# Kernel tuning notes

Measured on AMD Instinct MI355X. Metric: run time of the kernel, lower is better.

The kernel has to match this reference:

```python
import jax, jax.numpy as jnp
import numpy as np

N, E, H = 100000, 1250000, 64
NF, EF = 16, 3
BN_EPS = 1e-5
HALF = H // 2


def setup_inputs() -> dict:
    key = jax.random.key(0)
    ks = jax.random.split(key, 24)
    g = lambda i, shape, s=0.05: jax.random.normal(ks[i], shape, dtype=jnp.float32) * s
    return {
        "x": jax.random.normal(ks[0], (N, NF), dtype=jnp.float32),
        "edge_attr": jax.random.normal(ks[1], (E, EF), dtype=jnp.float32),
        "edge_index": jax.random.randint(ks[2], (2, E), 0, N),
        "W_node": g(3, (NF, H)), "b_node": g(4, (H,)),
        "W_edge": g(5, (EF, H)), "b_edge": g(6, (H,)),
        "W_lin0": g(7, (H, H)), "b_lin0": g(8, (H,)),
        "W_att0": g(9, (2 * H + EF, 1)), "b_att0": g(10, (1,)),
        "W_sage_l": g(11, (H, H)), "b_sage_l": g(12, (H,)),
        "W_sage_r": g(13, (H, H)),
        "W_gcn": g(14, (H, H)), "b_gcn": g(15, (H,)),
        "bn_gamma": jnp.ones((3, H), jnp.float32),
        "bn_beta": jnp.zeros((3, H), jnp.float32),
        "W_r1": g(16, (H, H)), "b_r1": g(17, (H,)),
        "W_r2": g(18, (H, HALF)), "b_r2": g(19, (HALF,)),
        "W_r3": g(20, (HALF, 1)), "b_r3": g(21, (1,)),
    }


def _bn_eval(x, gamma, beta):
    # eval-mode BatchNorm1d with running_mean=0, running_var=1
    return x * (gamma / jnp.sqrt(1.0 + BN_EPS)) + beta


def _edge_att(h, src, dst, edge_attr, W, b, Wa, ba):
    # EdgeAttentionLayer: lin -> per-edge attention MLP -> scatter-add at dst
    h = h @ W + b                                   # [N,H]
    hi, hj = h[dst], h[src]                         # [E,H] gathers
    a = jnp.concatenate([hi, hj, edge_attr], -1) @ Wa + ba   # [E,1]
    a = jax.nn.sigmoid(jax.nn.leaky_relu(a, 0.01))
    return jax.ops.segment_sum(hj * a, dst, num_segments=N)


def _sage(h, src, dst, Wl, bl, Wr):
    # SAGEConv (mean aggregation): lin_l(mean_j x_j) + lin_r(x)
    agg = jax.ops.segment_sum(h[src], dst, num_segments=N)
    cnt = jax.ops.segment_sum(jnp.ones((src.shape[0], 1), h.dtype), dst, num_segments=N)
    mean = agg / jnp.maximum(cnt, 1.0)
    return mean @ Wl + bl + h @ Wr


def _gcn(h, src, dst, W, b):
    # GCNConv with self-loops and symmetric normalization
    hw = h @ W
    loop = jnp.arange(N)
    s = jnp.concatenate([src, loop])
    d = jnp.concatenate([dst, loop])
    deg = jax.ops.segment_sum(jnp.ones(s.shape[0], hw.dtype), d, num_segments=N)
    dis = jnp.where(deg > 0, jax.lax.rsqrt(jnp.maximum(deg, 1.0)), 0.0)
    norm = dis[s] * dis[d]                          # [E+N]
    return jax.ops.segment_sum(hw[s] * norm[:, None], d, num_segments=N) + b


def reference(x, edge_attr, edge_index, W_node, b_node, W_edge, b_edge,
              W_lin0, b_lin0, W_att0, b_att0, W_sage_l, b_sage_l, W_sage_r,
              W_gcn, b_gcn, bn_gamma, bn_beta, W_r1, b_r1, W_r2, b_r2, W_r3, b_r3):
    src, dst = edge_index[0], edge_index[1]
    h = x @ W_node + b_node
    _unused = edge_attr @ W_edge + b_edge  # computed in original forward, never used

    # layer 0: EdgeAttentionLayer + BN + ReLU (+residual; eval dropout = identity)
    ident = h
    h = _edge_att(h, src, dst, edge_attr, W_lin0, b_lin0, W_att0, b_att0)
    h = jax.nn.relu(_bn_eval(h, bn_gamma[0], bn_beta[0])) + ident

    # layer 1: SAGEConv
    ident = h
    h = _sage(h, src, dst, W_sage_l, b_sage_l, W_sage_r)
    h = jax.nn.relu(_bn_eval(h, bn_gamma[1], bn_beta[1])) + ident

    # layer 2: GCNConv
    ident = h
    h = _gcn(h, src, dst, W_gcn, b_gcn)
    h = jax.nn.relu(_bn_eval(h, bn_gamma[2], bn_beta[2])) + ident

    h = jax.nn.relu(h @ W_r1 + b_r1)
    h = jax.nn.relu(h @ W_r2 + b_r2)
    return h @ W_r3 + b_r3  # [N,1]
```

## Files before the change

kernel.cpp:

```cpp
#include <hip/hip_runtime.h>
#include <hip/hip_fp16.h>
#include <math.h>

#define NODES 100000
#define EDGES 1250000
#define HD 64
#define NFD 16
#define CHUNK 1024
#define NCHUNK ((NODES + CHUNK - 1) / CHUNK)
#define BN_INV 0.9999950000374996f
#define LP 65
#define SRCMASK 0x1FFFFu
#define WSCALE (1.0f / 32768.0f)


__global__ void k_hist(const int* __restrict__ ei, int* __restrict__ deg) {
  int e = blockIdx.x * blockDim.x + threadIdx.x;
  if (e < EDGES) atomicAdd(&deg[ei[EDGES + e]], 1);
}

__global__ void k_scan1(const int* __restrict__ deg, int* __restrict__ part) {
  __shared__ int lds[256];
  int t = threadIdx.x, b = blockIdx.x;
  int base = b * CHUNK + t * 4;
  int s = 0;
#pragma unroll
  for (int m = 0; m < 4; m++) { int i = base + m; if (i < NODES) s += deg[i]; }
  lds[t] = s; __syncthreads();
  for (int off = 128; off > 0; off >>= 1) {
    if (t < off) lds[t] += lds[t + off];
    __syncthreads();
  }
  if (t == 0) part[b] = lds[0];
}

__global__ void k_scan2(int* __restrict__ part) {
  if (threadIdx.x == 0 && blockIdx.x == 0) {
    int run = 0;
    for (int c = 0; c < NCHUNK; c++) { int v = part[c]; part[c] = run; run += v; }
  }
}

__global__ void k_scan3(const int* __restrict__ deg, const int* __restrict__ part,
                        int* __restrict__ rowptr, int* __restrict__ cur,
                        float* __restrict__ dis) {
  __shared__ int lds[256];
  int t = threadIdx.x, b = blockIdx.x;
  int base = b * CHUNK + t * 4;
  int dl[4]; int s = 0;
#pragma unroll
  for (int m = 0; m < 4; m++) { int i = base + m; dl[m] = (i < NODES) ? deg[i] : 0; s += dl[m]; }
  lds[t] = s; __syncthreads();
  for (int off = 1; off < 256; off <<= 1) {
    int add = (t >= off) ? lds[t - off] : 0;
    __syncthreads();
    lds[t] += add;
    __syncthreads();
  }
  int run = part[b] + lds[t] - s;
#pragma unroll
  for (int m = 0; m < 4; m++) {
    int i = base + m;
    if (i < NODES) {
      rowptr[i] = run; cur[i] = run;
      dis[i] = 1.0f / sqrtf((float)(dl[m] + 1));
    }
    run += dl[m];
  }
  if (b == 0 && t == 0) rowptr[NODES] = EDGES;
}

__global__ void k_fillatt(const int* __restrict__ ei, const float* __restrict__ ea,
                          const float* __restrict__ cvec, const float* __restrict__ dvec,
                          const float* __restrict__ Wa, const float* __restrict__ ba,
                          int* __restrict__ cur, uint* __restrict__ sa) {
  int e = blockIdx.x * blockDim.x + threadIdx.x;
  if (e >= EDGES) return;
  int s = ei[e], d = ei[EDGES + e];
  float alin = cvec[d] + dvec[s] + ea[3 * e] * Wa[128] + ea[3 * e + 1] * Wa[129] +
               ea[3 * e + 2] * Wa[130] + ba[0];
  float lr = alin >= 0.f ? alin : 0.01f * alin;
  float a = 1.f / (1.f + expf(-lr));
  uint q = min((int)(a * 32768.f + 0.5f), 32767);
  int p = atomicAdd(&cur[d], 1);
  sa[p] = (q << 17) | (uint)s;
}


__device__ __forceinline__ void store16h(__half* dst, const float* v) {
  uint u[8];
#pragma unroll
  for (int j = 0; j < 8; j++) {
    __half2 h = __float22half2_rn(make_float2(v[2 * j], v[2 * j + 1]));
    u[j] = *reinterpret_cast<uint*>(&h);
  }
  uint4* o = (uint4*)dst;
  o[0] = make_uint4(u[0], u[1], u[2], u[3]);
  o[1] = make_uint4(u[4], u[5], u[6], u[7]);
}

__device__ __forceinline__ float4 h4tof4(uint2 u) {
  float2 fa = __half22float2(*reinterpret_cast<__half2*>(&u.x));
  float2 fb = __half22float2(*reinterpret_cast<__half2*>(&u.y));
  return make_float4(fa.x, fa.y, fb.x, fb.y);
}

__device__ __forceinline__ void gstep(const __half* __restrict__ tab,
                                      const uint* __restrict__ sa,
                                      int m, int end, int last, int sub, int col,
                                      bool weighted,
                                      float4& A0, float4& A1, float4& A2, float4& A3) {
  int e0 = m + sub, e1 = e0 + 4, e2 = e0 + 8, e3 = e0 + 12;
  uint s0 = sa[min(e0, last)], s1 = sa[min(e1, last)];
  uint s2 = sa[min(e2, last)], s3 = sa[min(e3, last)];
  float w0 = (e0 < end) ? (weighted ? (float)(s0 >> 17) * WSCALE : 1.f) : 0.f;
  float w1 = (e1 < end) ? (weighted ? (float)(s1 >> 17) * WSCALE : 1.f) : 0.f;
  float w2 = (e2 < end) ? (weighted ? (float)(s2 >> 17) * WSCALE : 1.f) : 0.f;
  float w3 = (e3 < end) ? (weighted ? (float)(s3 >> 17) * WSCALE : 1.f) : 0.f;
  uint2 u0 = *((const uint2*)(tab + (size_t)(s0 & SRCMASK) * HD) + col);
  uint2 u1 = *((const uint2*)(tab + (size_t)(s1 & SRCMASK) * HD) + col);
  uint2 u2 = *((const uint2*)(tab + (size_t)(s2 & SRCMASK) * HD) + col);
  uint2 u3 = *((const uint2*)(tab + (size_t)(s3 & SRCMASK) * HD) + col);
  {
    float4 f = h4tof4(u0);
    A0.x = fmaf(w0, f.x, A0.x); A0.y = fmaf(w0, f.y, A0.y);
    A0.z = fmaf(w0, f.z, A0.z); A0.w = fmaf(w0, f.w, A0.w);
  }
  {
    float4 f = h4tof4(u1);
    A1.x = fmaf(w1, f.x, A1.x); A1.y = fmaf(w1, f.y, A1.y);
    A1.z = fmaf(w1, f.z, A1.z); A1.w = fmaf(w1, f.w, A1.w);
  }
  {
    float4 f = h4tof4(u2);
    A2.x = fmaf(w2, f.x, A2.x); A2.y = fmaf(w2, f.y, A2.y);
    A2.z = fmaf(w2, f.z, A2.z); A2.w = fmaf(w2, f.w, A2.w);
  }
  {
    float4 f = h4tof4(u3);
    A3.x = fmaf(w3, f.x, A3.x); A3.y = fmaf(w3, f.y, A3.y);
    A3.z = fmaf(w3, f.z, A3.z); A3.w = fmaf(w3, f.w, A3.w);
  }
}

__device__ __forceinline__ float4 red4(float4 a0, float4 a1, float4 a2, float4 a3) {
  float4 r;
  r.x = (a0.x + a1.x) + (a2.x + a3.x);
  r.y = (a0.y + a1.y) + (a2.y + a3.y);
  r.z = (a0.z + a1.z) + (a2.z + a3.z);
  r.w = (a0.w + a1.w) + (a2.w + a3.w);
#pragma unroll
  for (int off = 16; off <= 32; off <<= 1) {
    r.x += __shfl_xor(r.x, off); r.y += __shfl_xor(r.y, off);
    r.z += __shfl_xor(r.z, off); r.w += __shfl_xor(r.w, off);
  }
  return r;
}

#define AGG_BODY16(TABLE, WEIGHTED)                                              \
  float4 acc0 = make_float4(0.f, 0.f, 0.f, 0.f);                                 \
  float4 acc1 = make_float4(0.f, 0.f, 0.f, 0.f);                                 \
  float4 acc2 = make_float4(0.f, 0.f, 0.f, 0.f);                                 \
  float4 acc3 = make_float4(0.f, 0.f, 0.f, 0.f);                                 \
  int last = end - 1;                                                            \
  for (int m = start; m < end; m += 16)                                          \
    gstep(TABLE, sa, m, end, last, sub, col, WEIGHTED, acc0, acc1, acc2, acc3);  \
  float4 accr = red4(acc0, acc1, acc2, acc3);


__global__ __launch_bounds__(256) void k_lin0(
    const float* __restrict__ x,
    const float* __restrict__ Wn, const float* __restrict__ bn,
    const float* __restrict__ Wl, const float* __restrict__ bl,
    const float* __restrict__ Wa,
    float* __restrict__ hA, __half* __restrict__ hB16,
    float* __restrict__ cvec, float* __restrict__ dvec) {
  __shared__ float sh[64 * LP];
  __shared__ float sc[4][64], sd[4][64];
  int slot = threadIdx.x & 63;
  int cc = __builtin_amdgcn_readfirstlane(threadIdx.x >> 6);
  int c0 = cc * 16;
  int n0 = blockIdx.x * 64 + slot;
  bool valid = n0 < NODES;
  int n = valid ? n0 : NODES - 1;
  const float4* xr = (const float4*)(x + (size_t)n * NFD);
  float acc[16];
#pragma unroll
  for (int j = 0; j < 16; j++) acc[j] = bn[c0 + j];
#pragma unroll
  for (int q = 0; q < 4; q++) {
    float4 xa = xr[q];
    float xs[4] = {xa.x, xa.y, xa.z, xa.w};
#pragma unroll
    for (int t = 0; t < 4; t++)
#pragma unroll
      for (int j = 0; j < 16; j++)
        acc[j] = fmaf(xs[t], Wn[(q * 4 + t) * HD + c0 + j], acc[j]);
  }
#pragma unroll
  for (int j = 0; j < 16; j++) sh[slot * LP + c0 + j] = acc[j];
  if (valid) {
    float4* o = (float4*)(hA + (size_t)n * HD + c0);
    o[0] = make_float4(acc[0], acc[1], acc[2], acc[3]);
    o[1] = make_float4(acc[4], acc[5], acc[6], acc[7]);
    o[2] = make_float4(acc[8], acc[9], acc[10], acc[11]);
    o[3] = make_float4(acc[12], acc[13], acc[14], acc[15]);
  }
  __syncthreads();
  float a2[16];
#pragma unroll
  for (int j = 0; j < 16; j++) a2[j] = bl[c0 + j];
#pragma unroll 8
  for (int k = 0; k < 64; k++) {
    float hk = sh[slot * LP + k];
#pragma unroll
    for (int j = 0; j < 16; j++)
      a2[j] = fmaf(hk, Wl[k * HD + c0 + j], a2[j]);
  }
  float cn = 0.f, dn = 0.f;
#pragma unroll
  for (int j = 0; j < 16; j++) {
    cn = fmaf(a2[j], Wa[c0 + j], cn);
    dn = fmaf(a2[j], Wa[64 + c0 + j], dn);
  }
  if (valid) store16h(hB16 + (size_t)n * HD + c0, a2);
  sc[cc][slot] = cn;
  sd[cc][slot] = dn;
  __syncthreads();
  if (cc == 0 && valid) {
    cvec[n] = sc[0][slot] + sc[1][slot] + sc[2][slot] + sc[3][slot];
    dvec[n] = sd[0][slot] + sd[1][slot] + sd[2][slot] + sd[3][slot];
  }
}

__global__ __launch_bounds__(256) void k_agg_att(
    const uint* __restrict__ sa, const int* __restrict__ rowptr,
    const float* __restrict__ hA, const __half* __restrict__ hB16,
    const float* __restrict__ g, const float* __restrict__ bt,
    float* __restrict__ hC, __half* __restrict__ hC16) {
  int lane = threadIdx.x & 63;
  int node = __builtin_amdgcn_readfirstlane(blockIdx.x * 4 + (threadIdx.x >> 6));
  if (node >= NODES) return;
  int start = rowptr[node], end = rowptr[node + 1];
  int sub = lane >> 4, col = lane & 15;
  float4 gg = ((const float4*)g)[col];
  float4 bb = ((const float4*)bt)[col];
  float4 ha = *((const float4*)(hA + (size_t)node * HD) + col);
  AGG_BODY16(hB16, true)
  if (lane < 16) {
    float4 v;
    v.x = fmaxf(accr.x * (gg.x * BN_INV) + bb.x, 0.f) + ha.x;
    v.y = fmaxf(accr.y * (gg.y * BN_INV) + bb.y, 0.f) + ha.y;
    v.z = fmaxf(accr.z * (gg.z * BN_INV) + bb.z, 0.f) + ha.z;
    v.w = fmaxf(accr.w * (gg.w * BN_INV) + bb.w, 0.f) + ha.w;
    *((float4*)(hC + (size_t)node * HD) + col) = v;
    __half2 p0 = __float22half2_rn(make_float2(v.x, v.y));
    __half2 p1 = __float22half2_rn(make_float2(v.z, v.w));
    uint2 u;
    u.x = *reinterpret_cast<uint*>(&p0);
    u.y = *reinterpret_cast<uint*>(&p1);
    *((uint2*)(hC16 + (size_t)node * HD) + col) = u;
  }
}

__global__ __launch_bounds__(256) void k_msage(
    const uint* __restrict__ sa, const int* __restrict__ rowptr,
    const float* __restrict__ hC, const __half* __restrict__ hC16,
    const float* __restrict__ Wl, const float* __restrict__ bl,
    const float* __restrict__ Wr, const float* __restrict__ Wg,
    const float* __restrict__ g, const float* __restrict__ bt,
    const float* __restrict__ dis,
    float* __restrict__ hA, __half* __restrict__ hD16) {
  __shared__ float sh[64 * LP];
  int lane = threadIdx.x & 63;
  int wu = __builtin_amdgcn_readfirstlane(threadIdx.x >> 6);
  int sub = lane >> 4, col = lane & 15;
  int nbase = blockIdx.x * 64;
  for (int i = 0; i < 16; i++) {
    int slot = wu * 16 + i;
    int nn = min(nbase + slot, NODES - 1);
    int start = rowptr[nn], end = rowptr[nn + 1];
    float rdeg = 1.f / fmaxf((float)(end - start), 1.f);
    AGG_BODY16(hC16, false)
    if (lane < 16) {
      sh[slot * LP + col * 4 + 0] = accr.x * rdeg;
      sh[slot * LP + col * 4 + 1] = accr.y * rdeg;
      sh[slot * LP + col * 4 + 2] = accr.z * rdeg;
      sh[slot * LP + col * 4 + 3] = accr.w * rdeg;
    }
  }
  __syncthreads();
  int c0 = wu * 16;
  int n0 = nbase + lane;
  bool valid = n0 < NODES;
  int n = valid ? n0 : NODES - 1;
  const float4* cr = (const float4*)(hC + (size_t)n * HD);
  float acc[16];
#pragma unroll
  for (int j = 0; j < 16; j++) acc[j] = bl[c0 + j];
#pragma unroll 8
  for (int k = 0; k < 64; k++) {
    float mk = sh[lane * LP + k];
#pragma unroll
    for (int j = 0; j < 16; j++)
      acc[j] = fmaf(mk, Wl[k * HD + c0 + j], acc[j]);
  }
#pragma unroll 4
  for (int q = 0; q < 16; q++) {
    float4 ac = cr[q];
    float cs[4] = {ac.x, ac.y, ac.z, ac.w};
#pragma unroll
    for (int t = 0; t < 4; t++)
#pragma unroll
      for (int j = 0; j < 16; j++)
        acc[j] = fmaf(cs[t], Wr[(q * 4 + t) * HD + c0 + j], acc[j]);
  }
  float tv[16];
  {
    float4 r0 = cr[wu * 4 + 0], r1 = cr[wu * 4 + 1], r2 = cr[wu * 4 + 2], r3 = cr[wu * 4 + 3];
    float rv[16] = {r0.x, r0.y, r0.z, r0.w, r1.x, r1.y, r1.z, r1.w,
                    r2.x, r2.y, r2.z, r2.w, r3.x, r3.y, r3.z, r3.w};
#pragma unroll
    for (int j = 0; j < 16; j++)
      tv[j] = fmaxf(acc[j] * (g[c0 + j] * BN_INV) + bt[c0 + j], 0.f) + rv[j];
  }
  __syncthreads();
#pragma unroll
  for (int j = 0; j < 16; j++) sh[lane * LP + c0 + j] = tv[j];
  if (valid) {
    float4* o = (float4*)(hA + (size_t)n * HD + c0);
    o[0] = make_float4(tv[0], tv[1], tv[2], tv[3]);
    o[1] = make_float4(tv[4], tv[5], tv[6], tv[7]);
    o[2] = make_float4(tv[8], tv[9], tv[10], tv[11]);
    o[3] = make_float4(tv[12], tv[13], tv[14], tv[15]);
  }
  __syncthreads();
  float di = dis[n];
  float a2[16];
#pragma unroll
  for (int j = 0; j < 16; j++) a2[j] = 0.f;
#pragma unroll 8
  for (int k = 0; k < 64; k++) {
    float tk = sh[lane * LP + k];
#pragma unroll
    for (int j = 0; j < 16; j++)
      a2[j] = fmaf(tk, Wg[k * HD + c0 + j], a2[j]);
  }
#pragma unroll
  for (int j = 0; j < 16; j++) a2[j] *= di;
  if (valid) store16h(hD16 + (size_t)n * HD + c0, a2);
}

__global__ __launch_bounds__(256) void k_gcnreg(
    const uint* __restrict__ sa, const int* __restrict__ rowptr,
    const float* __restrict__ dis,
    const float* __restrict__ hA,
    const __half* __restrict__ hD16,
    const float* __restrict__ bg,
    const float* __restrict__ g, const float* __restrict__ bt,
    const float* __restrict__ W1, const float* __restrict__ b1,
    const float* __restrict__ W2, const float* __restrict__ b2,
    const float* __restrict__ W3, const float* __restrict__ b3,
    float* __restrict__ out) {
  __shared__ float sh[64 * LP];
  __shared__ float sred[4][64];
  int lane = threadIdx.x & 63;
  int wu = __builtin_amdgcn_readfirstlane(threadIdx.x >> 6);
  int sub = lane >> 4, col = lane & 15;
  int nbase = blockIdx.x * 64;
  float4 gg = ((const float4*)g)[col];
  float4 bb = ((const float4*)bt)[col];
  float4 bgv = ((const float4*)bg)[col];
  for (int i = 0; i < 16; i++) {
    int slot = wu * 16 + i;
    int nn = min(nbase + slot, NODES - 1);
    int start = rowptr[nn], end = rowptr[nn + 1];
    float di = dis[nn];
    float4 sv = h4tof4(*((const uint2*)(hD16 + (size_t)nn * HD) + col));
    float4 ha = *((const float4*)(hA + (size_t)nn * HD) + col);
    AGG_BODY16(hD16, false)
    if (lane < 16) {
      sh[slot * LP + col * 4 + 0] =
          fmaxf((di * (accr.x + sv.x) + bgv.x) * (gg.x * BN_INV) + bb.x, 0.f) + ha.x;
      sh[slot * LP + col * 4 + 1] =
          fmaxf((di * (accr.y + sv.y) + bgv.y) * (gg.y * BN_INV) + bb.y, 0.f) + ha.y;
      sh[slot * LP + col * 4 + 2] =
          fmaxf((di * (accr.z + sv.z) + bgv.z) * (gg.z * BN_INV) + bb.z, 0.f) + ha.z;
      sh[slot * LP + col * 4 + 3] =
          fmaxf((di * (accr.w + sv.w) + bgv.w) * (gg.w * BN_INV) + bb.w, 0.f) + ha.w;
    }
  }
  __syncthreads();
  int c0 = wu * 16;
  int n0 = nbase + lane;
  bool valid = n0 < NODES;
  int n = valid ? n0 : NODES - 1;
  float acc[16];
#pragma unroll
  for (int j = 0; j < 16; j++) acc[j] = b1[c0 + j];
#pragma unroll 8
  for (int k = 0; k < 64; k++) {
    float rk = sh[lane * LP + k];
#pragma unroll
    for (int j = 0; j < 16; j++)
      acc[j] = fmaf(rk, W1[k * HD + c0 + j], acc[j]);
  }
  float t1v[16];
#pragma unroll
  for (int j = 0; j < 16; j++) t1v[j] = fmaxf(acc[j], 0.f);
  __syncthreads();
#pragma unroll
  for (int j = 0; j < 16; j++) sh[lane * LP + c0 + j] = t1v[j];
  __syncthreads();
  int d0 = wu * 8;
  float a2[8];
#pragma unroll
  for (int j = 0; j < 8; j++) a2[j] = b2[d0 + j];
#pragma unroll 8
  for (int k = 0; k < 64; k++) {
    float tk = sh[lane * LP + k];
#pragma unroll
    for (int j = 0; j < 8; j++)
      a2[j] = fmaf(tk, W2[k * 32 + d0 + j], a2[j]);
  }
  float part = 0.f;
#pragma unroll
  for (int j = 0; j < 8; j++) part = fmaf(fmaxf(a2[j], 0.f), W3[d0 + j], part);
  sred[wu][lane] = part;
  __syncthreads();
  if (wu == 0 && valid)
    out[n] = sred[0][lane] + sred[1][lane] + sred[2][lane] + sred[3][lane] + b3[0];
}


extern "C" void kernel_launch(void* const* d_in, const int* in_sizes, int n_in,
                              void* d_out, int out_size, void* d_ws, size_t ws_size,
                              hipStream_t stream) {
  const float* x      = (const float*)d_in[0];
  const float* ea     = (const float*)d_in[1];
  const int*   ei     = (const int*)d_in[2];
  const float* W_node = (const float*)d_in[3];
  const float* b_node = (const float*)d_in[4];
  const float* W_lin0 = (const float*)d_in[7];
  const float* b_lin0 = (const float*)d_in[8];
  const float* W_att0 = (const float*)d_in[9];
  const float* b_att0 = (const float*)d_in[10];
  const float* W_sl   = (const float*)d_in[11];
  const float* b_sl   = (const float*)d_in[12];
  const float* W_sr   = (const float*)d_in[13];
  const float* W_gcn  = (const float*)d_in[14];
  const float* b_gcn  = (const float*)d_in[15];
  const float* bn_g   = (const float*)d_in[16];
  const float* bn_b   = (const float*)d_in[17];
  const float* W_r1   = (const float*)d_in[18];
  const float* b_r1   = (const float*)d_in[19];
  const float* W_r2   = (const float*)d_in[20];
  const float* b_r2   = (const float*)d_in[21];
  const float* W_r3   = (const float*)d_in[22];
  const float* b_r3   = (const float*)d_in[23];
  float* out = (float*)d_out;

  char* ws = (char*)d_ws;
  size_t o = 0;
  auto alloc = [&](size_t bytes) -> void* {
    void* p = ws + o;
    o += (bytes + 255) & ~(size_t)255;
    return p;
  };
  int*    deg    = (int*)alloc(NODES * 4);
  int*    rowptr = (int*)alloc((NODES + 1) * 4);
  int*    cur    = (int*)alloc(NODES * 4);
  int*    part   = (int*)alloc(256 * 4);
  uint*   sa     = (uint*)alloc((size_t)EDGES * 4);
  float*  hA     = (float*)alloc((size_t)NODES * HD * 4);
  float*  hC     = (float*)alloc((size_t)NODES * HD * 4);
  __half* hB16   = (__half*)alloc((size_t)NODES * HD * 2);
  __half* hC16   = (__half*)alloc((size_t)NODES * HD * 2);
  __half* hD16   = (__half*)alloc((size_t)NODES * HD * 2);
  float*  cvec   = (float*)alloc(NODES * 4);
  float*  dvec   = (float*)alloc(NODES * 4);
  float*  dis    = (float*)alloc(NODES * 4);
  (void)ws_size; (void)in_sizes; (void)n_in; (void)out_size;

  const int EB  = (EDGES + 255) / 256;
  const int NT  = (NODES + 63) / 64;
  const int NBW = (NODES + 3) / 4;

  hipMemsetAsync(deg, 0, NODES * 4, stream);
  k_hist<<<EB, 256, 0, stream>>>(ei, deg);
  k_scan1<<<NCHUNK, 256, 0, stream>>>(deg, part);
  k_scan2<<<1, 64, 0, stream>>>(part);
  k_scan3<<<NCHUNK, 256, 0, stream>>>(deg, part, rowptr, cur, dis);

  k_lin0<<<NT, 256, 0, stream>>>(x, W_node, b_node, W_lin0, b_lin0, W_att0,
                                 hA, hB16, cvec, dvec);
  k_fillatt<<<EB, 256, 0, stream>>>(ei, ea, cvec, dvec, W_att0, b_att0, cur, sa);
  k_agg_att<<<NBW, 256, 0, stream>>>(sa, rowptr, hA, hB16,
                                     bn_g + 0 * HD, bn_b + 0 * HD, hC, hC16);
  k_msage<<<NT, 256, 0, stream>>>(sa, rowptr, hC, hC16, W_sl, b_sl, W_sr, W_gcn,
                                  bn_g + 1 * HD, bn_b + 1 * HD, dis, hA, hD16);
  k_gcnreg<<<NT, 256, 0, stream>>>(sa, rowptr, dis, hA, hD16, b_gcn,
                                   bn_g + 2 * HD, bn_b + 2 * HD,
                                   W_r1, b_r1, W_r2, b_r2, W_r3, b_r3, out);
}
```

Measured before the change: 312.7 us.

## Split SAGE mean aggregation into its own one-node-per-wave kernel

The fused SAGE kernel, where each wave serially aggregated 16 nodes before the dense matmuls, is split in two. A new kernel does the mean neighbor aggregation with one wave per node and writes fp16 means to a scratch buffer (reusing hB16). A second kernel loads those means into LDS and does the SAGE linear layers, batch norm, residual and GCN pre-transform. This gives the gather-bound aggregation much more parallelism and latency hiding, at the cost of an extra launch and an extra fp16 round trip through global memory.

```diff
diff --git a/kernel.cpp b/kernel.cpp
--- a/kernel.cpp
+++ b/kernel.cpp
@@ -263,44 +263,59 @@
   }
 }
 
-__global__ __launch_bounds__(256) void k_msage(
+__global__ __launch_bounds__(256) void k_agg_mean16(
     const uint* __restrict__ sa, const int* __restrict__ rowptr,
-    const float* __restrict__ hC, const __half* __restrict__ hC16,
+    const __half* __restrict__ hC16, __half* __restrict__ hM16) {
+  int lane = threadIdx.x & 63;
+  int node = __builtin_amdgcn_readfirstlane(blockIdx.x * 4 + (threadIdx.x >> 6));
+  if (node >= NODES) return;
+  int start = rowptr[node], end = rowptr[node + 1];
+  int sub = lane >> 4, col = lane & 15;
+  AGG_BODY16(hC16, false)
+  if (lane < 16) {
+    float rdeg = 1.f / fmaxf((float)(end - start), 1.f);
+    __half2 p0 = __float22half2_rn(make_float2(accr.x * rdeg, accr.y * rdeg));
+    __half2 p1 = __float22half2_rn(make_float2(accr.z * rdeg, accr.w * rdeg));
+    uint2 u;
+    u.x = *reinterpret_cast<uint*>(&p0);
+    u.y = *reinterpret_cast<uint*>(&p1);
+    *((uint2*)(hM16 + (size_t)node * HD) + col) = u;
+  }
+}
+
+__global__ __launch_bounds__(256) void k_sagegcn(
+    const __half* __restrict__ hM16, const float* __restrict__ hC,
     const float* __restrict__ Wl, const float* __restrict__ bl,
     const float* __restrict__ Wr, const float* __restrict__ Wg,
     const float* __restrict__ g, const float* __restrict__ bt,
     const float* __restrict__ dis,
     float* __restrict__ hA, __half* __restrict__ hD16) {
   __shared__ float sh[64 * LP];
-  int lane = threadIdx.x & 63;
-  int wu = __builtin_amdgcn_readfirstlane(threadIdx.x >> 6);
-  int sub = lane >> 4, col = lane & 15;
-  int nbase = blockIdx.x * 64;
-  for (int i = 0; i < 16; i++) {
-    int slot = wu * 16 + i;
-    int nn = min(nbase + slot, NODES - 1);
-    int start = rowptr[nn], end = rowptr[nn + 1];
-    float rdeg = 1.f / fmaxf((float)(end - start), 1.f);
-    AGG_BODY16(hC16, false)
-    if (lane < 16) {
-      sh[slot * LP + col * 4 + 0] = accr.x * rdeg;
-      sh[slot * LP + col * 4 + 1] = accr.y * rdeg;
-      sh[slot * LP + col * 4 + 2] = accr.z * rdeg;
-      sh[slot * LP + col * 4 + 3] = accr.w * rdeg;
-    }
-  }
-  __syncthreads();
-  int c0 = wu * 16;
-  int n0 = nbase + lane;
+  int slot = threadIdx.x & 63;
+  int cc = __builtin_amdgcn_readfirstlane(threadIdx.x >> 6);
+  int c0 = cc * 16;
+  int n0 = blockIdx.x * 64 + slot;
   bool valid = n0 < NODES;
   int n = valid ? n0 : NODES - 1;
+  {
+    const uint4* mp = (const uint4*)(hM16 + (size_t)n * HD + c0);
+    uint4 m0 = mp[0], m1 = mp[1];
+    uint mm[8] = {m0.x, m0.y, m0.z, m0.w, m1.x, m1.y, m1.z, m1.w};
+#pragma unroll
+    for (int j = 0; j < 8; j++) {
+      float2 f = __half22float2(*reinterpret_cast<__half2*>(&mm[j]));
+      sh[slot * LP + c0 + 2 * j] = f.x;
+      sh[slot * LP + c0 + 2 * j + 1] = f.y;
+    }
+  }
+  __syncthreads();
   const float4* cr = (const float4*)(hC + (size_t)n * HD);
   float acc[16];
 #pragma unroll
   for (int j = 0; j < 16; j++) acc[j] = bl[c0 + j];
 #pragma unroll 8
   for (int k = 0; k < 64; k++) {
-    float mk = sh[lane * LP + k];
+    float mk = sh[slot * LP + k];
 #pragma unroll
     for (int j = 0; j < 16; j++)
       acc[j] = fmaf(mk, Wl[k * HD + c0 + j], acc[j]);
@@ -317,7 +332,7 @@
   }
   float tv[16];
   {
-    float4 r0 = cr[wu * 4 + 0], r1 = cr[wu * 4 + 1], r2 = cr[wu * 4 + 2], r3 = cr[wu * 4 + 3];
+    float4 r0 = cr[cc * 4 + 0], r1 = cr[cc * 4 + 1], r2 = cr[cc * 4 + 2], r3 = cr[cc * 4 + 3];
     float rv[16] = {r0.x, r0.y, r0.z, r0.w, r1.x, r1.y, r1.z, r1.w,
                     r2.x, r2.y, r2.z, r2.w, r3.x, r3.y, r3.z, r3.w};
 #pragma unroll
@@ -326,7 +341,7 @@
   }
   __syncthreads();
 #pragma unroll
-  for (int j = 0; j < 16; j++) sh[lane * LP + c0 + j] = tv[j];
+  for (int j = 0; j < 16; j++) sh[slot * LP + c0 + j] = tv[j];
   if (valid) {
     float4* o = (float4*)(hA + (size_t)n * HD + c0);
     o[0] = make_float4(tv[0], tv[1], tv[2], tv[3]);
@@ -341,7 +356,7 @@
   for (int j = 0; j < 16; j++) a2[j] = 0.f;
 #pragma unroll 8
   for (int k = 0; k < 64; k++) {
-    float tk = sh[lane * LP + k];
+    float tk = sh[slot * LP + k];
 #pragma unroll
     for (int j = 0; j < 16; j++)
       a2[j] = fmaf(tk, Wg[k * HD + c0 + j], a2[j]);
@@ -497,8 +512,9 @@
   k_fillatt<<<EB, 256, 0, stream>>>(ei, ea, cvec, dvec, W_att0, b_att0, cur, sa);
   k_agg_att<<<NBW, 256, 0, stream>>>(sa, rowptr, hA, hB16,
                                      bn_g + 0 * HD, bn_b + 0 * HD, hC, hC16);
-  k_msage<<<NT, 256, 0, stream>>>(sa, rowptr, hC, hC16, W_sl, b_sl, W_sr, W_gcn,
-                                  bn_g + 1 * HD, bn_b + 1 * HD, dis, hA, hD16);
+  k_agg_mean16<<<NBW, 256, 0, stream>>>(sa, rowptr, hC16, hB16);
+  k_sagegcn<<<NT, 256, 0, stream>>>(hB16, hC, W_sl, b_sl, W_sr, W_gcn,
+                                    bn_g + 1 * HD, bn_b + 1 * HD, dis, hA, hD16);
   k_gcnreg<<<NT, 256, 0, stream>>>(sa, rowptr, dis, hA, hD16, b_gcn,
                                    bn_g + 2 * HD, bn_b + 2 * HD,
                                    W_r1, b_r1, W_r2, b_r2, W_r3, b_r3, out);
```

Result: no change. 308.9 us (-1.2%).
